# Performance work log

Measured on AMD Instinct MI355X. Metric: run time of the kernel, lower is better.

Reference implementation:

```python
import jax, jax.numpy as jnp
import numpy as np

B, T, D_IN, D_PROJ = 256, 2048, 25, 128


def setup_inputs() -> dict:
    key = jax.random.key(0)
    ks = jax.random.split(key, 7)
    s1 = 1.0 / np.sqrt(D_IN)
    s2 = 1.0 / np.sqrt(D_PROJ)
    return {
        "x": jax.random.normal(ks[0], (B, T, D_IN), dtype=jnp.float32),
        "ln_gamma": jnp.ones((D_IN,), dtype=jnp.float32),
        "ln_beta": jnp.zeros((D_IN,), dtype=jnp.float32),
        "w1": jax.random.uniform(ks[1], (D_IN, D_PROJ), jnp.float32, -s1, s1),
        "b1": jax.random.uniform(ks[2], (D_PROJ,), jnp.float32, -s1, s1),
        "w2": jax.random.uniform(ks[3], (D_PROJ, D_PROJ), jnp.float32, -s2, s2),
        "b2": jax.random.uniform(ks[4], (D_PROJ,), jnp.float32, -s2, s2),
    }


def reference(x, ln_gamma, ln_beta, w1, b1, w2, b2):
    # LayerNorm over last dim (eps=1e-5, torch default)
    mu = jnp.mean(x, axis=-1, keepdims=True)
    var = jnp.mean(jnp.square(x - mu), axis=-1, keepdims=True)
    xn = (x - mu) * jax.lax.rsqrt(var + 1e-5) * ln_gamma + ln_beta
    h = jnp.einsum("btd,dp->btp", xn, w1) + b1
    h = jax.nn.gelu(h, approximate=False)  # torch nn.GELU default = exact erf
    return jnp.einsum("btp,pq->btq", h, w2) + b2
```

## Files before the change

kernel.cpp:

```cpp
#include <hip/hip_runtime.h>
#include <hip/hip_bf16.h>
#include <stdint.h>

#define BT    (256*2048)
#define DIN   25
#define DP    128
#define MTILE 128
#define NBLK  (BT/MTILE)
#define HSTR  136

typedef __attribute__((ext_vector_type(8))) __bf16          bf16x8;
typedef __attribute__((ext_vector_type(8))) unsigned short  u16x8;
typedef __attribute__((ext_vector_type(4))) float           f32x4;

#define SM_H     0
#define SM_XN    34816
#define SM_SMALL (34816 + 8192)
#define SM_BYTES (SM_SMALL + 306*4)

__device__ __forceinline__ unsigned short f2bf(float f) {
  unsigned int u = __float_as_uint(f);
  u += 0x7fffu + ((u >> 16) & 1u);
  return (unsigned short)(u >> 16);
}

__device__ __forceinline__ float gelu_exact(float x) {
  float z  = 0.70710678118654752f * x;
  float az = __builtin_fabsf(z);
  float t  = __builtin_amdgcn_rcpf(1.0f + 0.3275911f * az);
  float p  = t*(0.254829592f + t*(-0.284496736f + t*(1.421413741f +
             t*(-1.453152027f + t*1.061405429f))));
  float e  = __expf(-z*z);
  float erf_az = 1.0f - p*e;
  float erf_z  = (x < 0.f) ? -erf_az : erf_az;
  return 0.5f * x * (1.0f + erf_z);
}

__device__ __forceinline__ void async16(void* lds, const void* g) {
  __builtin_amdgcn_global_load_lds(
      (const __attribute__((address_space(1))) unsigned int*)g,
      (__attribute__((address_space(3)))       unsigned int*)lds, 16, 0, 0);
}

__global__ void prep_kernel(const float* __restrict__ w1, const float* __restrict__ w2,
                            unsigned short* __restrict__ wf) {
  int idx = blockIdx.x * 256 + threadIdx.x;
  if (idx >= 40 * 512) return;
  int f = idx >> 9, r = idx & 511, l = r >> 3, j = r & 7;
  float val;
  if (f < 8) {
    int k = (l >> 4) * 8 + j;
    int n = f * 16 + (l & 15);
    val = (k < DIN) ? w1[k * DP + n] : 0.f;
  } else {
    int g = f - 8, nt = g >> 2, ks = g & 3;
    int k = ks * 32 + (l >> 4) * 8 + j;
    int n = nt * 16 + (l & 15);
    val = w2[k * DP + n];
  }
  wf[idx] = f2bf(val);
}

__global__ __launch_bounds__(256, 2) void fused_kernel(
    const float* __restrict__ x,   const float* __restrict__ gam,
    const float* __restrict__ bet, const float* __restrict__ b1,
    const float* __restrict__ b2,  const unsigned short* __restrict__ wfr,
    float* __restrict__ out) {
  __shared__ __align__(16) unsigned char smem[SM_BYTES];
  const int tid  = threadIdx.x;
  const int lane = tid & 63, w = tid >> 6;
  const int quad = lane >> 4, l15 = lane & 15;
  const long long row0 = (long long)blockIdx.x * MTILE;

  {
    const float* src = x + row0 * DIN;
    for (int c = tid; c < 800; c += 256)
      async16(smem + c * 16, src + c * 4);
  }
  float* sg  = (float*)(smem + SM_SMALL);
  float* sbt = sg + 25;
  float* sb1 = sbt + 25;
  float* sb2 = sb1 + 128;
  if (tid < 128) { sb1[tid] = b1[tid]; sb2[tid] = b2[tid]; }
  if (tid < 25)  { sg[tid] = gam[tid]; sbt[tid] = bet[tid]; }
  __syncthreads();

  if (tid < MTILE) {
    const float* xr = (const float*)smem + tid * DIN;
    float s = 0.f;
#pragma unroll
    for (int j = 0; j < DIN; j++) s += xr[j];
    float mu = s * (1.f / DIN);
    float v = 0.f;
#pragma unroll
    for (int j = 0; j < DIN; j++) { float d = xr[j] - mu; v += d * d; }
    float inv = rsqrtf(v * (1.f / DIN) + 1e-5f);
    int mt = tid >> 4, mr = tid & 15;
    unsigned char* fb = smem + SM_XN + mt * 1024;
#pragma unroll
    for (int q = 0; q < 4; q++) {
      u16x8 pk;
#pragma unroll
      for (int j = 0; j < 8; j++) {
        int k = q * 8 + j;
        float val = (k < DIN) ? ((xr[k] - mu) * inv * sg[k] + sbt[k]) : 0.f;
        pk[j] = f2bf(val);
      }
      *(u16x8*)(fb + (mr + 16 * q) * 16) = pk;
    }
  }
  __syncthreads();

  const unsigned char* wfb = (const unsigned char*)wfr;
  bf16x8 wb1[8];
#pragma unroll
  for (int nt = 0; nt < 8; nt++)
    wb1[nt] = *(const bf16x8*)(wfb + nt * 1024 + lane * 16);

  unsigned short* hb = (unsigned short*)smem;
  const f32x4 zf = {0.f, 0.f, 0.f, 0.f};
#pragma unroll
  for (int mi = 0; mi < 2; mi++) {
    int mt = w * 2 + mi;
    bf16x8 a = *(const bf16x8*)(smem + SM_XN + mt * 1024 + lane * 16);
    f32x4 acc[8];
#pragma unroll
    for (int nt = 0; nt < 8; nt++)
      acc[nt] = __builtin_amdgcn_mfma_f32_16x16x32_bf16(a, wb1[nt], zf, 0, 0, 0);
#pragma unroll
    for (int nt = 0; nt < 8; nt++) {
      float bias = sb1[nt * 16 + l15];
      int col = nt * 16 + l15;
#pragma unroll
      for (int r = 0; r < 4; r++) {
        int row = mt * 16 + quad * 4 + r;
        float hp = acc[nt][r] + bias;
        hb[row * HSTR + col] = f2bf(gelu_exact(hp));
      }
    }
  }
  __syncthreads();

  bf16x8 wb2[2][4];
#pragma unroll
  for (int ni = 0; ni < 2; ni++)
#pragma unroll
    for (int ks = 0; ks < 4; ks++)
      wb2[ni][ks] = *(const bf16x8*)(wfb + 8192 + (((w * 2 + ni) * 4) + ks) * 1024 + lane * 16);

  float bias0 = sb2[(w * 2 + 0) * 16 + l15];
  float bias1 = sb2[(w * 2 + 1) * 16 + l15];

  for (int mt = 0; mt < 8; mt++) {
    f32x4 a0 = zf, a1 = zf;
    f32x4 acc0 = zf, acc1 = zf;
#pragma unroll
    for (int ks = 0; ks < 4; ks++) {
      bf16x8 af = *(const bf16x8*)(smem + (mt * 16 + l15) * (HSTR * 2) + ks * 64 + quad * 16);
      acc0 = __builtin_amdgcn_mfma_f32_16x16x32_bf16(af, wb2[0][ks], acc0, 0, 0, 0);
      acc1 = __builtin_amdgcn_mfma_f32_16x16x32_bf16(af, wb2[1][ks], acc1, 0, 0, 0);
    }
    float* orow = out + (row0 + mt * 16) * DP;
    int c0 = (w * 2 + 0) * 16 + l15;
    int c1 = (w * 2 + 1) * 16 + l15;
#pragma unroll
    for (int r = 0; r < 4; r++) {
      int row = quad * 4 + r;
      orow[row * DP + c0] = acc0[r] + bias0;
      orow[row * DP + c1] = acc1[r] + bias1;
    }
    (void)a0; (void)a1;
  }
}

extern "C" void kernel_launch(void* const* d_in, const int* in_sizes, int n_in,
                              void* d_out, int out_size, void* d_ws, size_t ws_size,
                              hipStream_t stream) {
  const float* x   = (const float*)d_in[0];
  const float* gam = (const float*)d_in[1];
  const float* bet = (const float*)d_in[2];
  const float* w1  = (const float*)d_in[3];
  const float* b1  = (const float*)d_in[4];
  const float* w2  = (const float*)d_in[5];
  const float* b2  = (const float*)d_in[6];
  float* out = (float*)d_out;
  unsigned short* wf = (unsigned short*)d_ws;

  prep_kernel<<<80, 256, 0, stream>>>(w1, w2, wf);
  fused_kernel<<<NBLK, 256, 0, stream>>>(x, gam, bet, b1, b2, wf, out);
}
```

Measured before the change: 328.1 us.

## Make each wave own its 32 rows end-to-end, removing block barriers

Each wave now loads and normalizes its own 32 rows. LayerNorm runs directly in MFMA fragment layout using cross-lane shuffles, and the wave keeps its hidden activations in a private LDS region, so all __syncthreads are gone. The second GEMM loops over all 8 column tiles, streaming W2 fragments from global/L2 instead of holding a per-wave column slice. Launch bounds rise to 4 blocks per CU to raise occupancy. In exchange, each wave reloads the full W2 per tile, which adds global/L2 traffic and register pressure.

```diff
diff --git a/kernel.cpp b/kernel.cpp
--- a/kernel.cpp
+++ b/kernel.cpp
@@ -8,15 +8,13 @@
 #define MTILE 128
 #define NBLK  (BT/MTILE)
 #define HSTR  136
+#define WREG  (32*HSTR*2)
+#define XOFF  4608
+#define SM_BYTES (4*WREG)
 
 typedef __attribute__((ext_vector_type(8))) __bf16          bf16x8;
 typedef __attribute__((ext_vector_type(8))) unsigned short  u16x8;
 typedef __attribute__((ext_vector_type(4))) float           f32x4;
-
-#define SM_H     0
-#define SM_XN    34816
-#define SM_SMALL (34816 + 8192)
-#define SM_BYTES (SM_SMALL + 306*4)
 
 __device__ __forceinline__ unsigned short f2bf(float f) {
   unsigned int u = __float_as_uint(f);
@@ -61,7 +59,7 @@
   wf[idx] = f2bf(val);
 }
 
-__global__ __launch_bounds__(256, 2) void fused_kernel(
+__global__ __launch_bounds__(256, 4) void fused_kernel(
     const float* __restrict__ x,   const float* __restrict__ gam,
     const float* __restrict__ bet, const float* __restrict__ b1,
     const float* __restrict__ b2,  const unsigned short* __restrict__ wfr,
@@ -70,106 +68,130 @@
   const int tid  = threadIdx.x;
   const int lane = tid & 63, w = tid >> 6;
   const int quad = lane >> 4, l15 = lane & 15;
-  const long long row0 = (long long)blockIdx.x * MTILE;
+  const int kbase = quad * 8;
+  const long long rowW = (long long)blockIdx.x * MTILE + w * 32;
+  unsigned char* wbase = smem + w * WREG;
+  const unsigned char* wfb = (const unsigned char*)wfr;
 
   {
-    const float* src = x + row0 * DIN;
-    for (int c = tid; c < 800; c += 256)
-      async16(smem + c * 16, src + c * 4);
-  }
-  float* sg  = (float*)(smem + SM_SMALL);
-  float* sbt = sg + 25;
-  float* sb1 = sbt + 25;
-  float* sb2 = sb1 + 128;
-  if (tid < 128) { sb1[tid] = b1[tid]; sb2[tid] = b2[tid]; }
-  if (tid < 25)  { sg[tid] = gam[tid]; sbt[tid] = bet[tid]; }
-  __syncthreads();
-
-  if (tid < MTILE) {
-    const float* xr = (const float*)smem + tid * DIN;
-    float s = 0.f;
-#pragma unroll
-    for (int j = 0; j < DIN; j++) s += xr[j];
-    float mu = s * (1.f / DIN);
-    float v = 0.f;
-#pragma unroll
-    for (int j = 0; j < DIN; j++) { float d = xr[j] - mu; v += d * d; }
-    float inv = rsqrtf(v * (1.f / DIN) + 1e-5f);
-    int mt = tid >> 4, mr = tid & 15;
-    unsigned char* fb = smem + SM_XN + mt * 1024;
-#pragma unroll
-    for (int q = 0; q < 4; q++) {
-      u16x8 pk;
-#pragma unroll
-      for (int j = 0; j < 8; j++) {
-        int k = q * 8 + j;
-        float val = (k < DIN) ? ((xr[k] - mu) * inv * sg[k] + sbt[k]) : 0.f;
-        pk[j] = f2bf(val);
-      }
-      *(u16x8*)(fb + (mr + 16 * q) * 16) = pk;
-    }
-  }
-  __syncthreads();
-
-  const unsigned char* wfb = (const unsigned char*)wfr;
+    const long long xoff0 = rowW * (DIN * 4);
+    const long long xmax  = (long long)BT * DIN * 4 - 16;
+#pragma unroll
+    for (int i = 0; i < 4; i++) {
+      long long off = xoff0 + (long long)(i * 64 + lane) * 16;
+      if (off > xmax) off = xmax;
+      async16(wbase + XOFF + i * 1024 + lane * 16, (const unsigned char*)x + off);
+    }
+  }
+
+  float gk[8], bk[8];
+#pragma unroll
+  for (int j = 0; j < 8; j++) {
+    int k = kbase + j;
+    bool v = (k < DIN);
+    gk[j] = v ? gam[k] : 0.f;
+    bk[j] = v ? bet[k] : 0.f;
+  }
   bf16x8 wb1[8];
 #pragma unroll
   for (int nt = 0; nt < 8; nt++)
     wb1[nt] = *(const bf16x8*)(wfb + nt * 1024 + lane * 16);
 
-  unsigned short* hb = (unsigned short*)smem;
+  asm volatile("s_waitcnt vmcnt(0)" ::: "memory");
+  __builtin_amdgcn_sched_barrier(0);
+
+  const float* xs = (const float*)(wbase + XOFF);
+  bf16x8 afrag[2];
+#pragma unroll
+  for (int t = 0; t < 2; t++) {
+    float xv[8];
+    float s = 0.f;
+#pragma unroll
+    for (int j = 0; j < 8; j++) {
+      int k = kbase + j;
+      float v = 0.f;
+      if (k < DIN) v = xs[(t * 16 + l15) * DIN + k];
+      xv[j] = v;
+      s += v;
+    }
+    s += __shfl_xor(s, 16);  s += __shfl_xor(s, 32);
+    float mu = s * (1.f / DIN);
+    float vv = 0.f;
+#pragma unroll
+    for (int j = 0; j < 8; j++) {
+      int k = kbase + j;
+      float d = (k < DIN) ? (xv[j] - mu) : 0.f;
+      vv += d * d;
+    }
+    vv += __shfl_xor(vv, 16); vv += __shfl_xor(vv, 32);
+    float inv = rsqrtf(vv * (1.f / DIN) + 1e-5f);
+    u16x8 pk;
+#pragma unroll
+    for (int j = 0; j < 8; j++)
+      pk[j] = f2bf((xv[j] - mu) * inv * gk[j] + bk[j]);
+    afrag[t] = __builtin_bit_cast(bf16x8, pk);
+  }
+
+  float b1v[8];
+#pragma unroll
+  for (int nt = 0; nt < 8; nt++) b1v[nt] = b1[nt * 16 + l15];
+
+  unsigned short* hb = (unsigned short*)wbase;
   const f32x4 zf = {0.f, 0.f, 0.f, 0.f};
 #pragma unroll
-  for (int mi = 0; mi < 2; mi++) {
-    int mt = w * 2 + mi;
-    bf16x8 a = *(const bf16x8*)(smem + SM_XN + mt * 1024 + lane * 16);
+  for (int t = 0; t < 2; t++) {
     f32x4 acc[8];
 #pragma unroll
     for (int nt = 0; nt < 8; nt++)
-      acc[nt] = __builtin_amdgcn_mfma_f32_16x16x32_bf16(a, wb1[nt], zf, 0, 0, 0);
+      acc[nt] = __builtin_amdgcn_mfma_f32_16x16x32_bf16(afrag[t], wb1[nt], zf, 0, 0, 0);
 #pragma unroll
     for (int nt = 0; nt < 8; nt++) {
-      float bias = sb1[nt * 16 + l15];
+      float bias = b1v[nt];
       int col = nt * 16 + l15;
 #pragma unroll
       for (int r = 0; r < 4; r++) {
-        int row = mt * 16 + quad * 4 + r;
-        float hp = acc[nt][r] + bias;
-        hb[row * HSTR + col] = f2bf(gelu_exact(hp));
+        int row = t * 16 + quad * 4 + r;
+        hb[row * HSTR + col] = f2bf(gelu_exact(acc[nt][r] + bias));
       }
     }
   }
-  __syncthreads();
-
-  bf16x8 wb2[2][4];
-#pragma unroll
-  for (int ni = 0; ni < 2; ni++)
+
+  asm volatile("s_waitcnt lgkmcnt(0)" ::: "memory");
+  __builtin_amdgcn_sched_barrier(0);
+
+  bf16x8 af[2][4];
+#pragma unroll
+  for (int t = 0; t < 2; t++)
 #pragma unroll
     for (int ks = 0; ks < 4; ks++)
-      wb2[ni][ks] = *(const bf16x8*)(wfb + 8192 + (((w * 2 + ni) * 4) + ks) * 1024 + lane * 16);
-
-  float bias0 = sb2[(w * 2 + 0) * 16 + l15];
-  float bias1 = sb2[(w * 2 + 1) * 16 + l15];
-
-  for (int mt = 0; mt < 8; mt++) {
+      af[t][ks] = *(const bf16x8*)((const unsigned char*)hb +
+                    (t * 16 + l15) * (HSTR * 2) + ks * 64 + quad * 16);
+
+  float b2v[8];
+#pragma unroll
+  for (int nt = 0; nt < 8; nt++) b2v[nt] = b2[nt * 16 + l15];
+
+  float* orow = out + rowW * DP;
+#pragma unroll
+  for (int nt = 0; nt < 8; nt++) {
+    bf16x8 wq[4];
+#pragma unroll
+    for (int ks = 0; ks < 4; ks++)
+      wq[ks] = *(const bf16x8*)(wfb + 8192 + (nt * 4 + ks) * 1024 + lane * 16);
     f32x4 a0 = zf, a1 = zf;
-    f32x4 acc0 = zf, acc1 = zf;
 #pragma unroll
     for (int ks = 0; ks < 4; ks++) {
-      bf16x8 af = *(const bf16x8*)(smem + (mt * 16 + l15) * (HSTR * 2) + ks * 64 + quad * 16);
-      acc0 = __builtin_amdgcn_mfma_f32_16x16x32_bf16(af, wb2[0][ks], acc0, 0, 0, 0);
-      acc1 = __builtin_amdgcn_mfma_f32_16x16x32_bf16(af, wb2[1][ks], acc1, 0, 0, 0);
-    }
-    float* orow = out + (row0 + mt * 16) * DP;
-    int c0 = (w * 2 + 0) * 16 + l15;
-    int c1 = (w * 2 + 1) * 16 + l15;
+      a0 = __builtin_amdgcn_mfma_f32_16x16x32_bf16(af[0][ks], wq[ks], a0, 0, 0, 0);
+      a1 = __builtin_amdgcn_mfma_f32_16x16x32_bf16(af[1][ks], wq[ks], a1, 0, 0, 0);
+    }
+    int col = nt * 16 + l15;
+    float bias = b2v[nt];
 #pragma unroll
     for (int r = 0; r < 4; r++) {
-      int row = quad * 4 + r;
-      orow[row * DP + c0] = acc0[r] + bias0;
-      orow[row * DP + c1] = acc1[r] + bias1;
-    }
-    (void)a0; (void)a1;
+      int rr = quad * 4 + r;
+      orow[(long long)(rr)      * DP + col] = a0[r] + bias;
+      orow[(long long)(rr + 16) * DP + col] = a1[r] + bias;
+    }
   }
 }
 
```

Result: slower. 363.9 us (+10.9%).
